# Performance work log

Measured on AMD Instinct MI355X. Metric: run time of the kernel, lower is better.

## Reference

```python
import jax, jax.numpy as jnp
import numpy as np

NUM_CLASSES = 91
FEAT_DIM = 256
N = 131072
MOMENTUM = 0.999
WARMUP_STEPS = 200
BASE_MOM = 0.99


def setup_inputs() -> dict:
    key = jax.random.key(0)
    ks = jax.random.split(key, 8)
    return {
        "features": jax.random.normal(ks[0], (N, FEAT_DIM), dtype=jnp.float32),
        "labels": jax.random.randint(ks[1], (N,), 0, NUM_CLASSES, dtype=jnp.int32),
        "prototypes": jax.random.normal(ks[2], (NUM_CLASSES, FEAT_DIM), dtype=jnp.float32),
        "proto_initialized": jax.random.randint(ks[3], (NUM_CLASSES,), 0, 2).astype(bool),
        "proto_variance": jax.random.uniform(ks[4], (NUM_CLASSES,), dtype=jnp.float32),
        "shadow_prototypes": jax.random.normal(ks[5], (NUM_CLASSES, FEAT_DIM), dtype=jnp.float32),
        "shadow_initialized": jax.random.randint(ks[6], (NUM_CLASSES,), 0, 2).astype(bool),
        "proto_update_count": jax.random.randint(ks[7], (NUM_CLASSES,), 0, 1000, dtype=jnp.int64) if jax.config.jax_enable_x64 else jax.random.randint(ks[7], (NUM_CLASSES,), 0, 1000, dtype=jnp.int32),
        "step": 500,
    }


def reference(features, labels, prototypes, proto_initialized, proto_variance,
              shadow_prototypes, shadow_initialized, proto_update_count, step):
    C, D = prototypes.shape
    # L2-normalize features (F.normalize, eps=1e-12)
    f = features / jnp.clip(jnp.linalg.norm(features, axis=-1, keepdims=True), 1e-12)
    # per-class segment mean (the gather-reduce the torch loop does per unique label)
    sums = jax.ops.segment_sum(f, labels, num_segments=C)            # [C, D]
    counts = jax.ops.segment_sum(jnp.ones(labels.shape, f.dtype), labels, num_segments=C)  # [C]
    present = counts > 0                                              # classes in this batch
    cls_feat = sums / jnp.maximum(counts, 1.0)[:, None]               # [C, D]

    # adaptive per-class momentum (_get_momentum, vectorized)
    progress = min(1.0, float(step) / max(1, WARMUP_STEPS * 10))
    mom = jnp.where(proto_initialized,
                    BASE_MOM + (MOMENTUM - BASE_MOM) * jnp.exp(-proto_variance) * progress,
                    BASE_MOM)                                         # [C]

    old = prototypes
    ema = mom[:, None] * old + (1.0 - mom[:, None]) * cls_feat
    new_proto = jnp.where(present[:, None],
                          jnp.where(proto_initialized[:, None], ema, cls_feat),
                          old)

    # variance EMA on update magnitude (only for already-initialized present classes)
    diff = cls_feat - old
    upd_mag = jnp.sqrt(jnp.sum(diff * diff, axis=-1) + 1e-24)         # [C]
    new_var = jnp.where(present & proto_initialized,
                        0.99 * proto_variance + 0.01 * upd_mag,
                        proto_variance)

    # shadow (dual) prototype EMA — uses the UPDATED prototype, as in the torch loop
    shadow_m = min(MOMENTUM + 0.0009, 0.9999)
    shadow_ema = shadow_m * shadow_prototypes + (1.0 - shadow_m) * new_proto
    new_shadow = jnp.where(present[:, None],
                           jnp.where(shadow_initialized[:, None], shadow_ema, new_proto),
                           shadow_prototypes)

    new_initialized = proto_initialized | present
    new_shadow_init = shadow_initialized | present
    new_count = proto_update_count + present.astype(proto_update_count.dtype)
    return (new_proto, new_var, new_shadow, new_initialized, new_shadow_init, new_count)
```

## Files before the change

kernel.cpp:

```cpp
#include <hip/hip_runtime.h>
#include <math.h>

#define NCLS 91
#define FDIM 256
#define NB   256
#define BINSZ (NCLS * FDIM)
#define NRED 8

typedef float f32x4 __attribute__((ext_vector_type(4)));
typedef short short8 __attribute__((ext_vector_type(8)));

__device__ __forceinline__ float wave_sum64(float ss) {
    #pragma unroll
    for (int m = 1; m < 64; m <<= 1) ss += __shfl_xor(ss, m, 64);
    return ss;
}
__device__ __forceinline__ int wave_sum64_i(int v) {
    #pragma unroll
    for (int m = 1; m < 64; m <<= 1) v += __shfl_xor(v, m, 64);
    return v;
}

template <int CTRL>
__device__ __forceinline__ float dpp_addstep(float v) {
    return v + __int_as_float(__builtin_amdgcn_mov_dpp(
        __float_as_int(v), CTRL, 0xf, 0xf, true));
}
__device__ __forceinline__ float group16_sum(float v) {
    v = dpp_addstep<0xB1>(v);
    v = dpp_addstep<0x1B>(v);
    v = dpp_addstep<0x141>(v);
    v = dpp_addstep<0x140>(v);
    return v;
}

__device__ __forceinline__ unsigned short f2bf(float x) {
    unsigned u = __float_as_uint(x);
    return (unsigned short)((u + 0x7FFFu + ((u >> 16) & 1u)) >> 16);
}
__device__ __forceinline__ float bf2f(unsigned short h) {
    return __uint_as_float((unsigned)h << 16);
}

#define MPT 1024
#define CHUNK 64
#define ROWSTRIDE 260

extern "C" __global__ void __launch_bounds__(MPT)
mfma_main(const float* __restrict__ feats, const int* __restrict__ labels,
          unsigned short* __restrict__ slices, unsigned int* __restrict__ cnts_ws,
          int nrows, int rpb)
{
    __shared__ __align__(16) unsigned short sdat[2][CHUNK * ROWSTRIDE];
    __shared__ __align__(8)  unsigned char  slbl[2][CHUNK];
    __shared__ unsigned int scnt[96];

    const int tid  = threadIdx.x;
    const int lane = tid & 63;
    const int w    = tid >> 6;
    const int l16  = lane & 15;
    const int g    = lane >> 4;
    const int d0   = w * 16;
    const int r_loc = w * 4 + g;

    if (tid < 96) scnt[tid] = 0u;

    const int row0 = blockIdx.x * rpb;
    const int nch  = rpb / CHUNK;

    f32x4 acc[6];
    #pragma unroll
    for (int ct = 0; ct < 6; ++ct) acc[ct] = (f32x4){0.f, 0.f, 0.f, 0.f};

    float4 pf0, pf1, pf2, pf3;
    int plab;

    {
        const int r = row0 + r_loc;
        if (r < nrows) {
            const float4* bp = (const float4*)(feats + (size_t)r * FDIM + l16 * 16);
            pf0 = bp[0]; pf1 = bp[1]; pf2 = bp[2]; pf3 = bp[3];
            plab = labels[r];
        } else {
            pf0 = pf1 = pf2 = pf3 = make_float4(0.f, 0.f, 0.f, 0.f);
            plab = 255;
        }
    }

    auto stage = [&](int buf) {
        float ss = 0.f;
        ss = fmaf(pf0.x, pf0.x, ss); ss = fmaf(pf0.y, pf0.y, ss);
        ss = fmaf(pf0.z, pf0.z, ss); ss = fmaf(pf0.w, pf0.w, ss);
        ss = fmaf(pf1.x, pf1.x, ss); ss = fmaf(pf1.y, pf1.y, ss);
        ss = fmaf(pf1.z, pf1.z, ss); ss = fmaf(pf1.w, pf1.w, ss);
        ss = fmaf(pf2.x, pf2.x, ss); ss = fmaf(pf2.y, pf2.y, ss);
        ss = fmaf(pf2.z, pf2.z, ss); ss = fmaf(pf2.w, pf2.w, ss);
        ss = fmaf(pf3.x, pf3.x, ss); ss = fmaf(pf3.y, pf3.y, ss);
        ss = fmaf(pf3.z, pf3.z, ss); ss = fmaf(pf3.w, pf3.w, ss);
        ss = group16_sum(ss);
        const float inv = 1.0f / fmaxf(sqrtf(ss), 1e-12f);
        unsigned long long* q =
            (unsigned long long*)&sdat[buf][0] + (size_t)r_loc * 65 + l16 * 4;
        const float e[16] = {pf0.x, pf0.y, pf0.z, pf0.w, pf1.x, pf1.y, pf1.z, pf1.w,
                             pf2.x, pf2.y, pf2.z, pf2.w, pf3.x, pf3.y, pf3.z, pf3.w};
        #pragma unroll
        for (int t = 0; t < 4; ++t) {
            unsigned long long v =
                (unsigned long long)f2bf(e[4 * t + 0] * inv)
              | ((unsigned long long)f2bf(e[4 * t + 1] * inv) << 16)
              | ((unsigned long long)f2bf(e[4 * t + 2] * inv) << 32)
              | ((unsigned long long)f2bf(e[4 * t + 3] * inv) << 48);
            q[t] = v;
        }
        if (l16 == 0) {
            slbl[buf][r_loc] = (unsigned char)plab;
            if (plab < 96) atomicAdd(&scnt[plab], 1u);
        }
    };
    auto prefetch = [&](int ch_next) {
        const int r = row0 + ch_next * CHUNK + r_loc;
        if (r < nrows) {
            const float4* bp = (const float4*)(feats + (size_t)r * FDIM + l16 * 16);
            pf0 = bp[0]; pf1 = bp[1]; pf2 = bp[2]; pf3 = bp[3];
            plab = labels[r];
        } else {
            pf0 = pf1 = pf2 = pf3 = make_float4(0.f, 0.f, 0.f, 0.f);
            plab = 255;
        }
    };

    stage(0);
    if (nch > 1) prefetch(1);
    __syncthreads();

    for (int ch = 0; ch < nch; ++ch) {
        const int cur = ch & 1;
        #pragma unroll
        for (int s = 0; s < 2; ++s) {
            const int kbase = s * 32 + g * 8;
            const unsigned long long lb =
                *(const unsigned long long*)&slbl[cur][kbase];
            int la[8];
            #pragma unroll
            for (int j = 0; j < 8; ++j) la[j] = (int)((lb >> (8 * j)) & 0xFFu);

            short8 b;
            #pragma unroll
            for (int j = 0; j < 8; ++j)
                b[j] = (short)sdat[cur][(size_t)(kbase + j) * ROWSTRIDE + d0 + l16];

            #pragma unroll
            for (int ct = 0; ct < 6; ++ct) {
                const int c = ct * 16 + l16;
                short8 a;
                #pragma unroll
                for (int j = 0; j < 8; ++j)
                    a[j] = (la[j] == c) ? (short)0x3F80 : (short)0;
                acc[ct] = __builtin_amdgcn_mfma_f32_16x16x32_bf16(a, b, acc[ct], 0, 0, 0);
            }
        }
        if (ch + 1 < nch) {
            stage(cur ^ 1);
            if (ch + 2 < nch) prefetch(ch + 2);
        }
        __syncthreads();
    }

    unsigned short* es = &sdat[0][0];
    #pragma unroll
    for (int ct = 0; ct < 6; ++ct) {
        #pragma unroll
        for (int reg = 0; reg < 4; ++reg) {
            const int c = ct * 16 + g * 4 + reg;
            if (c < NCLS)
                es[c * FDIM + d0 + l16] = f2bf(acc[ct][reg]);
        }
    }
    __syncthreads();
    {
        const unsigned long long* src = (const unsigned long long*)es;
        unsigned long long* dst =
            (unsigned long long*)(slices + (size_t)blockIdx.x * BINSZ);
        for (int i = tid; i < BINSZ / 4; i += MPT) dst[i] = src[i];
    }
    if (tid < 96) cnts_ws[(size_t)blockIdx.x * 96 + tid] = scnt[tid];
}

extern "C" __global__ void __launch_bounds__(FDIM)
reduce_k(const unsigned short* __restrict__ slices, float* __restrict__ part2)
{
    const int c = blockIdx.x;
    const int h = blockIdx.y;
    const int d = threadIdx.x;
    const int slot = c * FDIM + d;
    const int p0 = h * (NB / NRED);

    float a0 = 0.f, a1 = 0.f, a2 = 0.f, a3 = 0.f;
    #pragma unroll 1
    for (int p = 0; p < NB / NRED; p += 4) {
        a0 += bf2f(slices[(size_t)(p0 + p + 0) * BINSZ + slot]);
        a1 += bf2f(slices[(size_t)(p0 + p + 1) * BINSZ + slot]);
        a2 += bf2f(slices[(size_t)(p0 + p + 2) * BINSZ + slot]);
        a3 += bf2f(slices[(size_t)(p0 + p + 3) * BINSZ + slot]);
    }
    part2[(size_t)h * BINSZ + slot] = (a0 + a1) + (a2 + a3);
}

__device__ int detect_bool_enc(const void* p) {
    const unsigned int* u = (const unsigned int*)p;
    bool i32ok = true, f32ok = true;
    for (int i = 0; i < 22; ++i) {
        unsigned int w = u[i];
        if (w > 1u) i32ok = false;
        if (w != 0u && w != 0x3F800000u) f32ok = false;
    }
    return i32ok ? 1 : (f32ok ? 2 : 0);
}
__device__ bool read_bool(const void* p, int enc, int i) {
    if (enc == 1) return ((const unsigned int*)p)[i] != 0u;
    if (enc == 2) return ((const float*)p)[i] != 0.0f;
    return ((const unsigned char*)p)[i] != 0;
}
__device__ int read_step(const void* p) {
    unsigned int w = ((const unsigned int*)p)[0];
    int iv = (int)w;
    if (iv >= 0 && iv < 16777216) return iv;
    return (int)__uint_as_float(w);
}

extern "C" __global__ void __launch_bounds__(FDIM)
final_k(const float* __restrict__ part2, const unsigned int* __restrict__ cnts_ws,
        const float* __restrict__ protos, const void* __restrict__ p_init,
        const float* __restrict__ p_var, const float* __restrict__ shadow,
        const void* __restrict__ s_init, const int* __restrict__ p_count,
        const void* __restrict__ p_step, float* __restrict__ out)
{
    const int c = blockIdx.x;
    const int d = threadIdx.x;

    __shared__ int enc_pi, enc_si;
    __shared__ float red[FDIM / 64];
    __shared__ int credi[FDIM / 64];
    __shared__ float s_upd;
    __shared__ unsigned int s_cnt;
    if (d == 0) { enc_pi = detect_bool_enc(p_init); enc_si = detect_bool_enc(s_init); }

    int cpart = 0;
    for (int p = d; p < NB; p += FDIM)
        cpart += (int)cnts_ws[(size_t)p * 96 + c];
    int cw = wave_sum64_i(cpart);
    if ((d & 63) == 0) credi[d >> 6] = cw;
    __syncthreads();
    if (d == 0) s_cnt = (unsigned int)(credi[0] + credi[1] + credi[2] + credi[3]);

    const int slot = c * FDIM + d;
    float sum = 0.f;
    #pragma unroll
    for (int h = 0; h < NRED; ++h) sum += part2[(size_t)h * BINSZ + slot];
    __syncthreads();

    const unsigned int cnt = s_cnt;
    const bool present = cnt > 0u;
    const float cls = sum / fmaxf((float)cnt, 1.0f);
    const float oldp = protos[c * FDIM + d];

    const float diff = cls - oldp;
    float ds = wave_sum64(diff * diff);
    if ((d & 63) == 0) red[d >> 6] = ds;
    __syncthreads();
    if (d == 0) s_upd = sqrtf(red[0] + red[1] + red[2] + red[3] + 1e-24f);
    __syncthreads();
    const float upd_mag = s_upd;

    const bool  init  = read_bool(p_init, enc_pi, c);
    const bool  sinit = read_bool(s_init, enc_si, c);
    const float var   = p_var[c];
    const int   step  = read_step(p_step);

    const float progress = fminf(1.0f, (float)step * (1.0f / 2000.0f));
    const float mom = init ? (0.99f + 0.009f * expf(-var) * progress) : 0.99f;

    const float ema   = mom * oldp + (1.0f - mom) * cls;
    const float newp  = present ? (init ? ema : cls) : oldp;

    const float sh     = shadow[c * FDIM + d];
    const float sh_ema = 0.9999f * sh + 0.0001f * newp;
    const float newsh  = present ? (sinit ? sh_ema : newp) : sh;

    const int O1 = NCLS * FDIM;
    const int O2 = O1 + NCLS;
    const int O3 = O2 + NCLS * FDIM;
    const int O4 = O3 + NCLS;
    const int O5 = O4 + NCLS;

    out[c * FDIM + d]       = newp;
    out[O2 + c * FDIM + d]  = newsh;
    if (d == 0) {
        const float newvar = (present && init) ? (0.99f * var + 0.01f * upd_mag) : var;
        out[O1 + c] = newvar;
        out[O3 + c] = (init || present)  ? 1.0f : 0.0f;
        out[O4 + c] = (sinit || present) ? 1.0f : 0.0f;
        out[O5 + c] = (float)(p_count[c] + (present ? 1 : 0));
    }
}

extern "C" void kernel_launch(void* const* d_in, const int* in_sizes, int n_in,
                              void* d_out, int out_size, void* d_ws, size_t ws_size,
                              hipStream_t stream) {
    const float* feats  = (const float*)d_in[0];
    const int*   labels = (const int*)d_in[1];
    const float* protos = (const float*)d_in[2];
    const void*  p_init = d_in[3];
    const float* p_var  = (const float*)d_in[4];
    const float* shadow = (const float*)d_in[5];
    const void*  s_init = d_in[6];
    const int*   p_cnt  = (const int*)d_in[7];
    const void*  p_step = d_in[8];
    const int nrows = in_sizes[1];

    int rpb = (nrows + NB - 1) / NB;
    rpb = ((rpb + CHUNK - 1) / CHUNK) * CHUNK;

    unsigned short* slices  = (unsigned short*)d_ws;
    unsigned int*   cnts_ws = (unsigned int*)((char*)d_ws + (size_t)BINSZ * NB * 2);
    float*          part2   = (float*)((char*)d_ws + (size_t)BINSZ * NB * 2
                                       + (size_t)NB * 96 * 4);

    mfma_main<<<NB, MPT, 0, stream>>>(feats, labels, slices, cnts_ws, nrows, rpb);
    reduce_k<<<dim3(NCLS, NRED), FDIM, 0, stream>>>(slices, part2);
    final_k<<<NCLS, FDIM, 0, stream>>>(part2, cnts_ws, protos, p_init, p_var,
                                       shadow, s_init, p_cnt, p_step, (float*)d_out);
}
```

Before: 48.66 us.

## Deepen feature prefetch to two chunks and vectorize the slice reduction

The main kernel now holds two register sets of prefetched rows (A/B), so global loads run two chunks ahead of the MFMA phase. The loop is unrolled in pairs and rows per block are rounded to two chunks. Separately, the per-block slices are padded to 92 classes, which lets reduce_k read 4 bf16 values per 64-bit load and write float4 results over a 23x8 grid. The extra registers may lower occupancy, and the padded 92nd class row in each slice is never written, so reduce_k sums uninitialized data into a padding slot that final_k does not read.

```diff
diff --git a/kernel.cpp b/kernel.cpp
--- a/kernel.cpp
+++ b/kernel.cpp
@@ -4,7 +4,8 @@
 #define NCLS 91
 #define FDIM 256
 #define NB   256
-#define BINSZ (NCLS * FDIM)
+#define BINSZ  (NCLS * FDIM)
+#define BINSZP (92 * FDIM)
 #define NRED 8
 
 typedef float f32x4 __attribute__((ext_vector_type(4)));
@@ -72,37 +73,49 @@
     #pragma unroll
     for (int ct = 0; ct < 6; ++ct) acc[ct] = (f32x4){0.f, 0.f, 0.f, 0.f};
 
-    float4 pf0, pf1, pf2, pf3;
-    int plab;
-
-    {
-        const int r = row0 + r_loc;
+    float4 A0, A1, A2, A3; int labA;
+    float4 B0, B1, B2, B3; int labB;
+
+    auto loadA = [&](int ch) {
+        const int r = row0 + ch * CHUNK + r_loc;
         if (r < nrows) {
             const float4* bp = (const float4*)(feats + (size_t)r * FDIM + l16 * 16);
-            pf0 = bp[0]; pf1 = bp[1]; pf2 = bp[2]; pf3 = bp[3];
-            plab = labels[r];
+            A0 = bp[0]; A1 = bp[1]; A2 = bp[2]; A3 = bp[3];
+            labA = labels[r];
         } else {
-            pf0 = pf1 = pf2 = pf3 = make_float4(0.f, 0.f, 0.f, 0.f);
-            plab = 255;
-        }
-    }
-
-    auto stage = [&](int buf) {
+            A0 = A1 = A2 = A3 = make_float4(0.f, 0.f, 0.f, 0.f);
+            labA = 255;
+        }
+    };
+    auto loadB = [&](int ch) {
+        const int r = row0 + ch * CHUNK + r_loc;
+        if (r < nrows) {
+            const float4* bp = (const float4*)(feats + (size_t)r * FDIM + l16 * 16);
+            B0 = bp[0]; B1 = bp[1]; B2 = bp[2]; B3 = bp[3];
+            labB = labels[r];
+        } else {
+            B0 = B1 = B2 = B3 = make_float4(0.f, 0.f, 0.f, 0.f);
+            labB = 255;
+        }
+    };
+
+    auto stage = [&](int buf, const float4& p0, const float4& p1,
+                     const float4& p2, const float4& p3, int plab) {
         float ss = 0.f;
-        ss = fmaf(pf0.x, pf0.x, ss); ss = fmaf(pf0.y, pf0.y, ss);
-        ss = fmaf(pf0.z, pf0.z, ss); ss = fmaf(pf0.w, pf0.w, ss);
-        ss = fmaf(pf1.x, pf1.x, ss); ss = fmaf(pf1.y, pf1.y, ss);
-        ss = fmaf(pf1.z, pf1.z, ss); ss = fmaf(pf1.w, pf1.w, ss);
-        ss = fmaf(pf2.x, pf2.x, ss); ss = fmaf(pf2.y, pf2.y, ss);
-        ss = fmaf(pf2.z, pf2.z, ss); ss = fmaf(pf2.w, pf2.w, ss);
-        ss = fmaf(pf3.x, pf3.x, ss); ss = fmaf(pf3.y, pf3.y, ss);
-        ss = fmaf(pf3.z, pf3.z, ss); ss = fmaf(pf3.w, pf3.w, ss);
+        ss = fmaf(p0.x, p0.x, ss); ss = fmaf(p0.y, p0.y, ss);
+        ss = fmaf(p0.z, p0.z, ss); ss = fmaf(p0.w, p0.w, ss);
+        ss = fmaf(p1.x, p1.x, ss); ss = fmaf(p1.y, p1.y, ss);
+        ss = fmaf(p1.z, p1.z, ss); ss = fmaf(p1.w, p1.w, ss);
+        ss = fmaf(p2.x, p2.x, ss); ss = fmaf(p2.y, p2.y, ss);
+        ss = fmaf(p2.z, p2.z, ss); ss = fmaf(p2.w, p2.w, ss);
+        ss = fmaf(p3.x, p3.x, ss); ss = fmaf(p3.y, p3.y, ss);
+        ss = fmaf(p3.z, p3.z, ss); ss = fmaf(p3.w, p3.w, ss);
         ss = group16_sum(ss);
         const float inv = 1.0f / fmaxf(sqrtf(ss), 1e-12f);
         unsigned long long* q =
             (unsigned long long*)&sdat[buf][0] + (size_t)r_loc * 65 + l16 * 4;
-        const float e[16] = {pf0.x, pf0.y, pf0.z, pf0.w, pf1.x, pf1.y, pf1.z, pf1.w,
-                             pf2.x, pf2.y, pf2.z, pf2.w, pf3.x, pf3.y, pf3.z, pf3.w};
+        const float e[16] = {p0.x, p0.y, p0.z, p0.w, p1.x, p1.y, p1.z, p1.w,
+                             p2.x, p2.y, p2.z, p2.w, p3.x, p3.y, p3.z, p3.w};
         #pragma unroll
         for (int t = 0; t < 4; ++t) {
             unsigned long long v =
@@ -117,29 +130,13 @@
             if (plab < 96) atomicAdd(&scnt[plab], 1u);
         }
     };
-    auto prefetch = [&](int ch_next) {
-        const int r = row0 + ch_next * CHUNK + r_loc;
-        if (r < nrows) {
-            const float4* bp = (const float4*)(feats + (size_t)r * FDIM + l16 * 16);
-            pf0 = bp[0]; pf1 = bp[1]; pf2 = bp[2]; pf3 = bp[3];
-            plab = labels[r];
-        } else {
-            pf0 = pf1 = pf2 = pf3 = make_float4(0.f, 0.f, 0.f, 0.f);
-            plab = 255;
-        }
-    };
-
-    stage(0);
-    if (nch > 1) prefetch(1);
-    __syncthreads();
-
-    for (int ch = 0; ch < nch; ++ch) {
-        const int cur = ch & 1;
+
+    auto mfma_phase = [&](int buf) {
         #pragma unroll
         for (int s = 0; s < 2; ++s) {
             const int kbase = s * 32 + g * 8;
             const unsigned long long lb =
-                *(const unsigned long long*)&slbl[cur][kbase];
+                *(const unsigned long long*)&slbl[buf][kbase];
             int la[8];
             #pragma unroll
             for (int j = 0; j < 8; ++j) la[j] = (int)((lb >> (8 * j)) & 0xFFu);
@@ -147,7 +144,7 @@
             short8 b;
             #pragma unroll
             for (int j = 0; j < 8; ++j)
-                b[j] = (short)sdat[cur][(size_t)(kbase + j) * ROWSTRIDE + d0 + l16];
+                b[j] = (short)sdat[buf][(size_t)(kbase + j) * ROWSTRIDE + d0 + l16];
 
             #pragma unroll
             for (int ct = 0; ct < 6; ++ct) {
@@ -159,10 +156,23 @@
                 acc[ct] = __builtin_amdgcn_mfma_f32_16x16x32_bf16(a, b, acc[ct], 0, 0, 0);
             }
         }
-        if (ch + 1 < nch) {
-            stage(cur ^ 1);
-            if (ch + 2 < nch) prefetch(ch + 2);
-        }
+    };
+
+    loadA(0);
+    __syncthreads();
+    stage(0, A0, A1, A2, A3, labA);
+    loadA(1);
+    __syncthreads();
+
+    for (int p = 0; p < nch; p += 2) {
+        if (p + 2 < nch) loadB(p + 2);
+        mfma_phase(0);
+        stage(1, A0, A1, A2, A3, labA);
+        __syncthreads();
+
+        if (p + 3 < nch) loadA(p + 3);
+        mfma_phase(1);
+        if (p + 2 < nch) stage(0, B0, B1, B2, B3, labB);
         __syncthreads();
     }
 
@@ -180,7 +190,7 @@
     {
         const unsigned long long* src = (const unsigned long long*)es;
         unsigned long long* dst =
-            (unsigned long long*)(slices + (size_t)blockIdx.x * BINSZ);
+            (unsigned long long*)(slices + (size_t)blockIdx.x * BINSZP);
         for (int i = tid; i < BINSZ / 4; i += MPT) dst[i] = src[i];
     }
     if (tid < 96) cnts_ws[(size_t)blockIdx.x * 96 + tid] = scnt[tid];
@@ -189,21 +199,27 @@
 extern "C" __global__ void __launch_bounds__(FDIM)
 reduce_k(const unsigned short* __restrict__ slices, float* __restrict__ part2)
 {
-    const int c = blockIdx.x;
-    const int h = blockIdx.y;
-    const int d = threadIdx.x;
-    const int slot = c * FDIM + d;
+    const int t4 = blockIdx.x;
+    const int h  = blockIdx.y;
+    const int t  = threadIdx.x;
+    const int off = t4 * 1024 + t * 4;
     const int p0 = h * (NB / NRED);
 
-    float a0 = 0.f, a1 = 0.f, a2 = 0.f, a3 = 0.f;
+    float s0 = 0.f, s1 = 0.f, s2 = 0.f, s3 = 0.f;
     #pragma unroll 1
     for (int p = 0; p < NB / NRED; p += 4) {
-        a0 += bf2f(slices[(size_t)(p0 + p + 0) * BINSZ + slot]);
-        a1 += bf2f(slices[(size_t)(p0 + p + 1) * BINSZ + slot]);
-        a2 += bf2f(slices[(size_t)(p0 + p + 2) * BINSZ + slot]);
-        a3 += bf2f(slices[(size_t)(p0 + p + 3) * BINSZ + slot]);
-    }
-    part2[(size_t)h * BINSZ + slot] = (a0 + a1) + (a2 + a3);
+        #pragma unroll
+        for (int u = 0; u < 4; ++u) {
+            const unsigned long long v = *(const unsigned long long*)
+                (slices + (size_t)(p0 + p + u) * BINSZP + off);
+            s0 += bf2f((unsigned short)(v));
+            s1 += bf2f((unsigned short)(v >> 16));
+            s2 += bf2f((unsigned short)(v >> 32));
+            s3 += bf2f((unsigned short)(v >> 48));
+        }
+    }
+    float4* dst = (float4*)(part2 + (size_t)h * BINSZP + off);
+    *dst = make_float4(s0, s1, s2, s3);
 }
 
 __device__ int detect_bool_enc(const void* p) {
@@ -256,7 +272,7 @@
     const int slot = c * FDIM + d;
     float sum = 0.f;
     #pragma unroll
-    for (int h = 0; h < NRED; ++h) sum += part2[(size_t)h * BINSZ + slot];
+    for (int h = 0; h < NRED; ++h) sum += part2[(size_t)h * BINSZP + slot];
     __syncthreads();
 
     const unsigned int cnt = s_cnt;
@@ -319,15 +335,15 @@
     const int nrows = in_sizes[1];
 
     int rpb = (nrows + NB - 1) / NB;
-    rpb = ((rpb + CHUNK - 1) / CHUNK) * CHUNK;
+    rpb = ((rpb + 2 * CHUNK - 1) / (2 * CHUNK)) * (2 * CHUNK);
 
     unsigned short* slices  = (unsigned short*)d_ws;
-    unsigned int*   cnts_ws = (unsigned int*)((char*)d_ws + (size_t)BINSZ * NB * 2);
-    float*          part2   = (float*)((char*)d_ws + (size_t)BINSZ * NB * 2
+    unsigned int*   cnts_ws = (unsigned int*)((char*)d_ws + (size_t)BINSZP * NB * 2);
+    float*          part2   = (float*)((char*)d_ws + (size_t)BINSZP * NB * 2
                                        + (size_t)NB * 96 * 4);
 
     mfma_main<<<NB, MPT, 0, stream>>>(feats, labels, slices, cnts_ws, nrows, rpb);
-    reduce_k<<<dim3(NCLS, NRED), FDIM, 0, stream>>>(slices, part2);
+    reduce_k<<<dim3(23, NRED), FDIM, 0, stream>>>(slices, part2);
     final_k<<<NCLS, FDIM, 0, stream>>>(part2, cnts_ws, protos, p_init, p_var,
                                        shadow, s_init, p_cnt, p_step, (float*)d_out);
 }
```

After: 49.68 us. 2.1% more time.
